# Kernel tuning notes

Measured on AMD Instinct MI355X. Metric: run time of the kernel, lower is better.

The kernel has to match this reference:

```python
import jax, jax.numpy as jnp
import numpy as np

N = 100000        # nodes
E = 3200000       # edges (avg degree 32)
D_IN, D_H, D_OUT = 128, 128, 64
EPS = 1e-5        # BatchNorm eps


def setup_inputs() -> dict:
    key = jax.random.key(0)
    ks = jax.random.split(key, 12)
    s = 0.1
    return {
        "x": jax.random.normal(ks[0], (N, D_IN), jnp.float32),
        "edge_index": jax.random.randint(ks[1], (2, E), 0, N, jnp.int32),
        "W1": jax.random.normal(ks[2], (D_IN, D_H), jnp.float32) * s,
        "b1": jnp.zeros((D_H,), jnp.float32),
        "W2": jax.random.normal(ks[3], (D_H, D_H), jnp.float32) * s,
        "b2": jnp.zeros((D_H,), jnp.float32),
        "W3": jax.random.normal(ks[4], (D_H, D_OUT), jnp.float32) * s,
        "b3": jnp.zeros((D_OUT,), jnp.float32),
        "g1": jnp.ones((D_H,), jnp.float32),
        "be1": jnp.zeros((D_H,), jnp.float32),
        "g2": jnp.ones((D_H,), jnp.float32),
        "be2": jnp.zeros((D_H,), jnp.float32),
    }


def reference(x, edge_index, W1, b1, W2, b2, W3, b3, g1, be1, g2, be2):
    # GCNConv normalization: add self-loops, symmetric deg^-1/2 A deg^-1/2
    loop = jnp.arange(N, dtype=edge_index.dtype)
    src = jnp.concatenate([edge_index[0], loop])   # [E+N]
    dst = jnp.concatenate([edge_index[1], loop])   # [E+N]
    deg = jax.ops.segment_sum(jnp.ones(src.shape, x.dtype), dst, num_segments=N)
    dinv = jnp.where(deg > 0, jax.lax.rsqrt(deg), 0.0)
    norm = (dinv[src] * dinv[dst])[:, None]        # [E+N, 1]

    def conv(h, W, b):
        h = h @ W                                   # dense transform [N, d]
        msg = h[src] * norm                         # gather + scale [E+N, d]
        return jax.ops.segment_sum(msg, dst, num_segments=N) + b

    def bn(h, g, be):  # BatchNorm1d over nodes (batch stats, eval-style dropout)
        m = h.mean(axis=0)
        v = h.var(axis=0)
        return (h - m) * jax.lax.rsqrt(v + EPS) * g + be

    h = jax.nn.relu(bn(conv(x, W1, b1), g1, be1))
    h = jax.nn.relu(bn(conv(h, W2, b2), g2, be2))
    h = conv(h, W3, b3)
    return jax.nn.softmax(h, axis=1)
```

## Files before the change

kernel.cpp:

```cpp
#include <hip/hip_runtime.h>
#include <hip/hip_fp16.h>

constexpr int   NN   = 100000;
constexpr int   NE   = 3200000;
constexpr float BN_EPS = 1e-5f;

constexpr int MG_B  = (NN / 32 + 3) / 4;
constexpr int NB    = (NN + 127) / 128;
constexpr int HB    = 256;
constexpr int CHUNK = NE / HB;
constexpr int BKT_CAP = 5120;
constexpr int IDXW = 512;
constexpr int NPAN = 8;

typedef _Float16 half8 __attribute__((ext_vector_type(8)));
typedef _Float16 h2v   __attribute__((ext_vector_type(2)));
typedef float    floatx16 __attribute__((ext_vector_type(16)));
typedef float    floatx8  __attribute__((ext_vector_type(8)));
typedef int      intx4   __attribute__((ext_vector_type(4)));


__device__ __forceinline__ void acc8_fdot2(floatx8& acc, half8 h) {
  h2v* p = (h2v*)&h;
  const h2v LO = {(_Float16)1.f, (_Float16)0.f};
  const h2v HI = {(_Float16)0.f, (_Float16)1.f};
#pragma unroll
  for (int j = 0; j < 4; ++j) {
    acc[2*j]   = __builtin_amdgcn_fdot2(p[j], LO, acc[2*j],   false);
    acc[2*j+1] = __builtin_amdgcn_fdot2(p[j], HI, acc[2*j+1], false);
  }
}

__global__ __launch_bounds__(256) void k_wprep_all(const float* __restrict__ W1,
                                                   const float* __restrict__ W2,
                                                   const float* __restrict__ W3,
                                                   _Float16* __restrict__ Wt1,
                                                   _Float16* __restrict__ Wt2,
                                                   _Float16* __restrict__ Wt3) {
  int idx = blockIdx.x * 256 + threadIdx.x;
  if (idx < 16384) {
    int k = idx >> 7, n = idx & 127;
    Wt1[n * 128 + k] = (_Float16)W1[idx];
  } else if (idx < 32768) {
    int j = idx - 16384, k = j >> 7, n = j & 127;
    Wt2[n * 128 + k] = (_Float16)W2[j];
  } else if (idx < 40960) {
    int j = idx - 32768, k = j >> 6, n = j & 63;
    Wt3[n * 128 + k] = (_Float16)W3[j];
  }
}

__global__ __launch_bounds__(256) void k_f1(const int* __restrict__ dst,
                                            int* __restrict__ blkhist,
                                            const float* __restrict__ x,
                                            const _Float16* __restrict__ Wt1,
                                            _Float16* __restrict__ C) {
  __shared__ int h[NB];
  if (blockIdx.x < MG_B) {
    int wid  = (blockIdx.x * 256 + threadIdx.x) >> 6;
    int lane = threadIdx.x & 63;
    if (wid >= NN / 32) return;
    const int m = lane & 31;
    const int q = lane >> 5;
    const int row0 = wid * 32;
    const float* Arow = x + (size_t)(row0 + m) * 128 + q * 8;

    floatx16 acc[4] = {};
#pragma unroll
    for (int s = 0; s < 8; ++s) {
      float4 a0 = *(const float4*)(Arow + 16 * s);
      float4 a1 = *(const float4*)(Arow + 16 * s + 4);
      half8 af;
      af[0] = (_Float16)a0.x; af[1] = (_Float16)a0.y;
      af[2] = (_Float16)a0.z; af[3] = (_Float16)a0.w;
      af[4] = (_Float16)a1.x; af[5] = (_Float16)a1.y;
      af[6] = (_Float16)a1.z; af[7] = (_Float16)a1.w;
#pragma unroll
      for (int ct = 0; ct < 4; ++ct) {
        half8 bf = *(const half8*)(Wt1 + (size_t)(ct * 32 + m) * 128 + q * 8 + 16 * s);
        acc[ct] = __builtin_amdgcn_mfma_f32_32x32x16_f16(af, bf, acc[ct], 0, 0, 0);
      }
    }
#pragma unroll
    for (int ct = 0; ct < 4; ++ct) {
      int p = ct * 2 + (m >> 4);
      int off = m & 15;
#pragma unroll
      for (int r = 0; r < 16; ++r) {
        int row = (r & 3) + 8 * (r >> 2) + 4 * q;
        C[((size_t)p * NN + row0 + row) * 16 + off] = (_Float16)acc[ct][r];
      }
    }
  } else {
    int j = blockIdx.x - MG_B;
    int t = threadIdx.x;
    for (int b = t; b < NB; b += 256) h[b] = 0;
    __syncthreads();
    int base = j * CHUNK;
    for (int e = base + t; e < base + CHUNK; e += 256)
      atomicAdd(&h[dst[e] >> 7], 1);
    __syncthreads();
    for (int b = t; b < NB; b += 256) blkhist[j * NB + b] = h[b];
  }
}

__global__ __launch_bounds__(256) void k_scan_bkt_a(const int* __restrict__ blkhist,
                                                    int* __restrict__ blkbase,
                                                    int* __restrict__ total) {
  int wid  = (blockIdx.x * 256 + threadIdx.x) >> 6;
  int lane = threadIdx.x & 63;
  if (wid >= NB) return;
  int i0 = lane * 4;
  int v0 = blkhist[(i0 + 0) * NB + wid];
  int v1 = blkhist[(i0 + 1) * NB + wid];
  int v2 = blkhist[(i0 + 2) * NB + wid];
  int v3 = blkhist[(i0 + 3) * NB + wid];
  int lt = v0 + v1 + v2 + v3;
  int inc = lt;
#pragma unroll
  for (int off = 1; off < 64; off <<= 1) {
    int xx = __shfl_up(inc, off);
    if (lane >= off) inc += xx;
  }
  int exc = inc - lt;
  blkbase[(i0 + 0) * NB + wid] = exc;
  blkbase[(i0 + 1) * NB + wid] = exc + v0;
  blkbase[(i0 + 2) * NB + wid] = exc + v0 + v1;
  blkbase[(i0 + 3) * NB + wid] = exc + v0 + v1 + v2;
  if (lane == 63) total[wid] = inc;
}

__global__ __launch_bounds__(1024) void k_scan_bkt_b(const int* __restrict__ total,
                                                     int* __restrict__ bbase) {
  __shared__ int s[1024];
  int t = threadIdx.x;
  int v = (t < NB) ? total[t] : 0;
  s[t] = v;
  __syncthreads();
  for (int off = 1; off < 1024; off <<= 1) {
    int xx = (t >= off) ? s[t - off] : 0;
    __syncthreads();
    s[t] += xx;
    __syncthreads();
  }
  if (t < NB) bbase[t] = s[t] - v;
  if (t == NB - 1) bbase[NB] = s[t];
}

__global__ __launch_bounds__(256) void k_scatter(const int* __restrict__ ei,
                                                 const int* __restrict__ bbase,
                                                 const int* __restrict__ blkbase,
                                                 int* __restrict__ ebuf) {
  __shared__ int cur[NB];
  int i = blockIdx.x;
  int t = threadIdx.x;
  for (int b = t; b < NB; b += 256) cur[b] = bbase[b] + blkbase[i * NB + b];
  __syncthreads();
  int base = i * CHUNK;
  for (int e = base + t; e < base + CHUNK; e += 256) {
    int s = ei[e];
    int d = ei[NE + e];
    int b = d >> 7;
    int pos = atomicAdd(&cur[b], 1);
    ebuf[pos] = s | ((d & 127) << 17);
  }
}

__global__ __launch_bounds__(256) void k_bucket(const int* __restrict__ bbase,
                                                const int* __restrict__ ebuf,
                                                int* __restrict__ rowptr,
                                                float* __restrict__ dinv,
                                                int* __restrict__ csrc,
                                                _Float16* __restrict__ Hf) {
  __shared__ int degL[128];
  __shared__ int sc[128];
  __shared__ int curL[128];
  __shared__ float dvs[128];
  __shared__ int sorted[BKT_CAP];
  int b = blockIdx.x;
  int t = threadIdx.x;
  int e0 = bbase[b], e1 = bbase[b + 1];
  int cnt = e1 - e0;
  if (t < 128) degL[t] = 0;
  __syncthreads();
  for (int e = e0 + t; e < e1; e += 256)
    atomicAdd(&degL[ebuf[e] >> 17], 1);
  __syncthreads();
  if (t < 128) sc[t] = degL[t];
  __syncthreads();
  for (int off = 1; off < 128; off <<= 1) {
    int xx = 0;
    if (t < 128 && t >= off) xx = sc[t - off];
    __syncthreads();
    if (t < 128) sc[t] += xx;
    __syncthreads();
  }
  if (t < 128) {
    int node = b * 128 + t;
    float dv = 0.f;
    if (node < NN) {
      int d = degL[t];
      int exc = sc[t] - d;
      rowptr[node] = e0 + exc;
      dv = rsqrtf((float)(d + 1));
      dinv[node] = dv;
      curL[t] = exc;
    }
    dvs[t] = dv;
  }
  if (b == NB - 1 && t == 0) rowptr[NN] = NE;
  __syncthreads();
  if (cnt <= BKT_CAP) {
    for (int e = e0 + t; e < e1; e += 256) {
      int p = ebuf[e];
      int pos = atomicAdd(&curL[p >> 17], 1);
      sorted[pos] = p & 0x1FFFF;
    }
    __syncthreads();
    for (int i = t; i < cnt; i += 256) csrc[e0 + i] = sorted[i];
  } else {
    for (int e = e0 + t; e < e1; e += 256) {
      int p = ebuf[e];
      int pos = atomicAdd(&curL[p >> 17], 1);
      csrc[e0 + pos] = p & 0x1FFFF;
    }
  }
  int node = b * 128 + (t >> 1);
  if (node < NN) {
    float dv = dvs[t >> 1];
    size_t base = (size_t)node * 16 + (t & 1) * 8;
#pragma unroll
    for (int k = 0; k < NPAN; ++k) {
      size_t a = (size_t)k * ((size_t)NN * 16) + base;
      half8 h = *(const half8*)(Hf + a);
#pragma unroll
      for (int j = 0; j < 8; ++j) h[j] = (_Float16)((float)h[j] * dv);
      *(half8*)(Hf + a) = h;
    }
  }
}

template <int BN_, bool POUT>
__global__ __launch_bounds__(256) void k_mgemm(const _Float16* __restrict__ A,
                                               const _Float16* __restrict__ Wt,
                                               const float* __restrict__ scale,
                                               const float* __restrict__ shift,
                                               const float* __restrict__ dinv,
                                               _Float16* __restrict__ C) {
  constexpr int NCT = BN_ / 32;
  int wid  = (blockIdx.x * 256 + threadIdx.x) >> 6;
  int lane = threadIdx.x & 63;
  if (wid >= NN / 32) return;
  const int m = lane & 31;
  const int q = lane >> 5;
  const int row0 = wid * 32;

  const _Float16* Abase = A + (size_t)(row0 + m) * 16 + q * 8;

  floatx16 acc[NCT] = {};

#pragma unroll
  for (int s = 0; s < 8; ++s) {
    half8 raw = *(const half8*)(Abase + (size_t)s * ((size_t)NN * 16));
    int k0 = 16 * s + q * 8;
    half8 af;
#pragma unroll
    for (int j = 0; j < 8; ++j) {
      float a = fmaxf(fmaf((float)raw[j], scale[k0 + j], shift[k0 + j]), 0.f);
      af[j] = (_Float16)a;
    }
#pragma unroll
    for (int ct = 0; ct < NCT; ++ct) {
      half8 bf = *(const half8*)(Wt + (size_t)(ct * 32 + m) * 128 + q * 8 + 16 * s);
      acc[ct] = __builtin_amdgcn_mfma_f32_32x32x16_f16(af, bf, acc[ct], 0, 0, 0);
    }
  }

#pragma unroll
  for (int ct = 0; ct < NCT; ++ct) {
    int p = ct * 2 + (m >> 4);
    int off = m & 15;
#pragma unroll
    for (int r = 0; r < 16; ++r) {
      int row = (r & 3) + 8 * (r >> 2) + 4 * q;
      float dv = dinv[row0 + row];
      _Float16 val = (_Float16)(acc[ct][r] * dv);
      if (POUT)
        C[((size_t)p * NN + row0 + row) * 16 + off] = val;
      else
        C[(size_t)(row0 + row) * BN_ + ct * 32 + m] = val;
    }
  }
}

__global__ __launch_bounds__(256) void k_agg128p(const _Float16* __restrict__ Hp,
                                                 const float* __restrict__ dinv,
                                                 const int* __restrict__ rowptr,
                                                 const int* __restrict__ srcs,
                                                 _Float16* __restrict__ outp) {
  __shared__ int sidx[4][IDXW];
  int p  = blockIdx.x & 7;
  int nb = blockIdx.x >> 3;
  int t  = threadIdx.x;
  int w    = t >> 6;
  int lane = t & 63;
  int nid  = lane >> 4;
  int slot = (lane >> 1) & 7;
  int half = lane & 1;
  int node = nb * 16 + w * 4 + nid;

  int beg = rowptr[node];
  int end = rowptr[node + 1];
  int w0   = __shfl(beg, 0);
  int wend = __shfl(end, 63);
  int cnt  = wend - w0;
  int* my = sidx[w];
  bool fits = (cnt <= IDXW);
  if (fits)
    for (int i = lane; i < cnt; i += 64) my[i] = srcs[w0 + i];

  int deg = end - beg;
  int nit = (deg + 7) >> 3;
  int mx = nit;
  mx = max(mx, __shfl_xor(mx, 16));
  mx = max(mx, __shfl_xor(mx, 32));

  const _Float16* base = Hp + (size_t)p * ((size_t)NN * 16) + half * 8;
  int lo = beg - w0;
  floatx8 acc = {};
  if (slot == 0) {
    half8 h = *(const half8*)(base + (size_t)node * 16);
    acc8_fdot2(acc, h);
  }

  int it = 0;
  for (; it + 2 <= mx; it += 2) {
    int j0 = it * 8 + slot;
    int j1 = j0 + 8;
    bool v0 = j0 < deg;
    bool v1 = j1 < deg;
    if (v0) {
      int r0 = fits ? my[lo + j0] : srcs[beg + j0];
      half8 h0 = *(const half8*)(base + (size_t)r0 * 16);
      acc8_fdot2(acc, h0);
    }
    if (v1) {
      int r1 = fits ? my[lo + j1] : srcs[beg + j1];
      half8 h1 = *(const half8*)(base + (size_t)r1 * 16);
      acc8_fdot2(acc, h1);
    }
  }
  for (; it < mx; ++it) {
    int j0 = it * 8 + slot;
    if (j0 < deg) {
      int r0 = fits ? my[lo + j0] : srcs[beg + j0];
      half8 h0 = *(const half8*)(base + (size_t)r0 * 16);
      acc8_fdot2(acc, h0);
    }
  }

#pragma unroll
  for (int k = 0; k < 8; ++k) {
    acc[k] += __shfl_xor(acc[k], 2);
    acc[k] += __shfl_xor(acc[k], 4);
    acc[k] += __shfl_xor(acc[k], 8);
  }
  if (slot == 0) {
    float di = dinv[node];
    __half2 o[4];
#pragma unroll
    for (int j = 0; j < 4; ++j)
      o[j] = __floats2half2_rn(acc[2 * j] * di, acc[2 * j + 1] * di);
    *(intx4*)(outp + ((size_t)p * NN + node) * 16 + half * 8) = *(const intx4*)o;
  }
}

__global__ __launch_bounds__(256) void k_agg64_softmax(const __half* __restrict__ H,
                                                       const float* __restrict__ dinv,
                                                       const int* __restrict__ rowptr,
                                                       const int* __restrict__ srcs,
                                                       const float* __restrict__ b3,
                                                       float* __restrict__ out) {
  int wid  = (blockIdx.x * 256 + threadIdx.x) >> 6;
  int lane = threadIdx.x & 63;
  if (wid >= NN) return;
  const int g  = lane >> 3;
  const int sl = lane & 7;
  const _Float16* Hb = (const _Float16*)H + (size_t)sl * 8;
  floatx8 acc = {};
  if (g == 0) {
    half8 h = *(const half8*)(Hb + (size_t)wid * 64);
    acc8_fdot2(acc, h);
  }
  int beg = rowptr[wid], end = rowptr[wid + 1];
  int n = end - beg;
  int chunk = (n + 7) >> 3;
  int e  = beg + g * chunk; if (e > end) e = end;
  int ce = e + chunk;       if (ce > end) ce = end;
  for (; e + 4 <= ce; e += 4) {
    int s0 = srcs[e + 0], s1 = srcs[e + 1];
    int s2 = srcs[e + 2], s3 = srcs[e + 3];
    half8 h0 = *(const half8*)(Hb + (size_t)s0 * 64);
    half8 h1 = *(const half8*)(Hb + (size_t)s1 * 64);
    half8 h2 = *(const half8*)(Hb + (size_t)s2 * 64);
    half8 h3 = *(const half8*)(Hb + (size_t)s3 * 64);
    acc8_fdot2(acc, h0);
    acc8_fdot2(acc, h1);
    acc8_fdot2(acc, h2);
    acc8_fdot2(acc, h3);
  }
  for (; e < ce; ++e) {
    half8 h0 = *(const half8*)(Hb + (size_t)srcs[e] * 64);
    acc8_fdot2(acc, h0);
  }
#pragma unroll
  for (int j = 0; j < 8; ++j) {
    acc[j] += __shfl_xor(acc[j], 8);
    acc[j] += __shfl_xor(acc[j], 16);
    acc[j] += __shfl_xor(acc[j], 32);
  }
  float di = dinv[wid];
  float4 bA = *(const float4*)(b3 + sl * 8);
  float4 bB = *(const float4*)(b3 + sl * 8 + 4);
  float v[8];
  v[0] = acc[0] * di + bA.x; v[1] = acc[1] * di + bA.y;
  v[2] = acc[2] * di + bA.z; v[3] = acc[3] * di + bA.w;
  v[4] = acc[4] * di + bB.x; v[5] = acc[5] * di + bB.y;
  v[6] = acc[6] * di + bB.z; v[7] = acc[7] * di + bB.w;
  float m = v[0];
#pragma unroll
  for (int j = 1; j < 8; ++j) m = fmaxf(m, v[j]);
  m = fmaxf(m, __shfl_xor(m, 1));
  m = fmaxf(m, __shfl_xor(m, 2));
  m = fmaxf(m, __shfl_xor(m, 4));
  float s = 0.f;
#pragma unroll
  for (int j = 0; j < 8; ++j) { v[j] = __expf(v[j] - m); s += v[j]; }
  s += __shfl_xor(s, 1);
  s += __shfl_xor(s, 2);
  s += __shfl_xor(s, 4);
  float inv = 1.0f / s;
  if (g == 0) {
    float4 oA = {v[0] * inv, v[1] * inv, v[2] * inv, v[3] * inv};
    float4 oB = {v[4] * inv, v[5] * inv, v[6] * inv, v[7] * inv};
    *(float4*)(out + (size_t)wid * 64 + sl * 8)     = oA;
    *(float4*)(out + (size_t)wid * 64 + sl * 8 + 4) = oB;
  }
}

__global__ __launch_bounds__(256) void k_stats(const __half2* __restrict__ H2,
                                               float* __restrict__ S1,
                                               float* __restrict__ S2) {
  int t = threadIdx.x;
  int cp = t & 63;
  int r = t >> 6;
  const __half2* Pb = H2 + (size_t)(cp >> 3) * ((size_t)NN * 8) + (cp & 7);
  float2 s1 = {0.f, 0.f}, s2 = {0.f, 0.f};
  for (int row = blockIdx.x * 4 + r; row < NN; row += gridDim.x * 4) {
    float2 v = __half22float2(Pb[(size_t)row * 8]);
    s1.x += v.x; s1.y += v.y;
    s2.x += v.x * v.x; s2.y += v.y * v.y;
  }
  __shared__ float2 l1[256], l2[256];
  l1[t] = s1; l2[t] = s2;
  __syncthreads();
  if (t < 128) {
    l1[t].x += l1[t+128].x; l1[t].y += l1[t+128].y;
    l2[t].x += l2[t+128].x; l2[t].y += l2[t+128].y;
  }
  __syncthreads();
  if (t < 64) {
    float2 a1 = l1[t], b1 = l1[t+64];
    float2 a2 = l2[t], b2 = l2[t+64];
    atomicAdd(&S1[2*cp+0], a1.x + b1.x);
    atomicAdd(&S1[2*cp+1], a1.y + b1.y);
    atomicAdd(&S2[2*cp+0], a2.x + b2.x);
    atomicAdd(&S2[2*cp+1], a2.y + b2.y);
  }
}

__global__ void k_finalize(const float* __restrict__ S1, const float* __restrict__ S2,
                           const float* __restrict__ g,  const float* __restrict__ be,
                           float* __restrict__ scale,    float* __restrict__ shift) {
  int t = threadIdx.x;
  float mean = S1[t] * (1.0f / NN);
  float var  = S2[t] * (1.0f / NN) - mean * mean;
  float is   = rsqrtf(var + BN_EPS);
  float sc   = g[t] * is;
  scale[t] = sc;
  shift[t] = be[t] - mean * sc;
}

extern "C" void kernel_launch(void* const* d_in, const int* in_sizes, int n_in,
                              void* d_out, int out_size, void* d_ws, size_t ws_size,
                              hipStream_t stream) {
  (void)in_sizes; (void)n_in; (void)out_size; (void)ws_size;
  const float* x   = (const float*)d_in[0];
  const int*   ei  = (const int*)d_in[1];
  const float* W1  = (const float*)d_in[2];
  const float* W2  = (const float*)d_in[4];
  const float* W3  = (const float*)d_in[6];
  const float* b3  = (const float*)d_in[7];
  const float* g1  = (const float*)d_in[8];
  const float* be1 = (const float*)d_in[9];
  const float* g2  = (const float*)d_in[10];
  const float* be2 = (const float*)d_in[11];
  float* out = (float*)d_out;

  char* ws = (char*)d_ws;
  size_t off = 0;
  auto take = [&](size_t bytes) -> char* {
    char* p = ws + off;
    off = (off + bytes + 255) & ~(size_t)255;
    return p;
  };
  float* S1a    = (float*)take(128 * 4);
  float* S2a    = (float*)take(128 * 4);
  float* S1b    = (float*)take(128 * 4);
  float* S2b    = (float*)take(128 * 4);
  size_t zero_bytes = off;
  float* scale1 = (float*)take(128 * 4);
  float* shift1 = (float*)take(128 * 4);
  float* scale2 = (float*)take(128 * 4);
  float* shift2 = (float*)take(128 * 4);
  float* dinv   = (float*)take((size_t)NN * 4);
  int*   rowptr = (int*)  take((size_t)(NN + 1) * 4);
  int*   bbase  = (int*)  take((size_t)(NB + 1) * 4);
  int*   total  = (int*)  take((size_t)NB * 4);
  int*   blkhist= (int*)  take((size_t)HB * NB * 4);
  int*   blkbase= (int*)  take((size_t)HB * NB * 4);
  int*   ebuf   = (int*)  take((size_t)NE * 4);
  int*   csrc   = (int*)  take((size_t)NE * 4);
  _Float16* Wt1 = (_Float16*)take((size_t)128 * 128 * 2);
  _Float16* Wt2 = (_Float16*)take((size_t)128 * 128 * 2);
  _Float16* Wt3 = (_Float16*)take((size_t)64 * 128 * 2);
  _Float16* Hf  = (_Float16*)take((size_t)NN * 128 * 2);
  _Float16* hB  = (_Float16*)take((size_t)NN * 128 * 2);

  (void)hipMemsetAsync(d_ws, 0, zero_bytes, stream);

  const int mgB  = MG_B;
  const int aggB = (NN + 3) / 4;
  const int aggPB = NPAN * (NN / 16);
  const int scanAB = (NB + 3) / 4;

  k_wprep_all<<<160, 256, 0, stream>>>(W1, W2, W3, Wt1, Wt2, Wt3);

  k_f1<<<MG_B + HB, 256, 0, stream>>>(ei + NE, blkhist, x, Wt1, Hf);

  k_scan_bkt_a<<<scanAB, 256, 0, stream>>>(blkhist, blkbase, total);
  k_scan_bkt_b<<<1, 1024, 0, stream>>>(total, bbase);
  k_scatter<<<HB, 256, 0, stream>>>(ei, bbase, blkbase, ebuf);
  k_bucket<<<NB, 256, 0, stream>>>(bbase, ebuf, rowptr, dinv, csrc, Hf);

  k_agg128p<<<aggPB, 256, 0, stream>>>(Hf, dinv, rowptr, csrc, hB);
  k_stats<<<1024, 256, 0, stream>>>((const __half2*)hB, S1a, S2a);
  k_finalize<<<1, 128, 0, stream>>>(S1a, S2a, g1, be1, scale1, shift1);

  k_mgemm<128, true><<<mgB, 256, 0, stream>>>(hB, Wt2, scale1, shift1, dinv, Hf);
  k_agg128p<<<aggPB, 256, 0, stream>>>(Hf, dinv, rowptr, csrc, hB);
  k_stats<<<1024, 256, 0, stream>>>((const __half2*)hB, S1b, S2b);
  k_finalize<<<1, 128, 0, stream>>>(S1b, S2b, g2, be2, scale2, shift2);

  k_mgemm<64, false><<<mgB, 256, 0, stream>>>(hB, Wt3, scale2, shift2, dinv, Hf);
  k_agg64_softmax<<<aggB, 256, 0, stream>>>((const __half*)Hf, dinv, rowptr, csrc, b3, out);
}
```

Before: 741.2 us.

## Assign eight nodes per wave in panel aggregation with contiguous per-slot edge ranges

The 128-wide panel aggregation kernel now maps 8 nodes per wavefront with 4 edge slots each, down from 4 nodes with 8 slots, and halves the grid. Each slot walks a contiguous chunk of the node's edge list with a 4-way unrolled gather, replacing the interleaved strided loop. This removes the wave-wide max-iteration loop and one shuffle reduction stage, and gives more independent loads in flight per lane. In exchange, load balance within a node is coarser and more edge indices share the per-wave shared-memory buffer, so more waves may fall back to global index reads.

```diff
diff --git a/kernel.cpp b/kernel.cpp
--- a/kernel.cpp
+++ b/kernel.cpp
@@ -304,13 +304,14 @@
   int t  = threadIdx.x;
   int w    = t >> 6;
   int lane = t & 63;
-  int nid  = lane >> 4;
-  int slot = (lane >> 1) & 7;
+  int nid  = lane >> 3;
+  int slot = (lane >> 1) & 3;
   int half = lane & 1;
-  int node = nb * 16 + w * 4 + nid;
+  int node = nb * 32 + w * 8 + nid;
 
   int beg = rowptr[node];
   int end = rowptr[node + 1];
+  int deg = end - beg;
   int w0   = __shfl(beg, 0);
   int wend = __shfl(end, 63);
   int cnt  = wend - w0;
@@ -319,42 +320,51 @@
   if (fits)
     for (int i = lane; i < cnt; i += 64) my[i] = srcs[w0 + i];
 
-  int deg = end - beg;
-  int nit = (deg + 7) >> 3;
-  int mx = nit;
-  mx = max(mx, __shfl_xor(mx, 16));
-  mx = max(mx, __shfl_xor(mx, 32));
+  int q  = (deg + 3) >> 2;
+  int e0 = slot * q; if (e0 > deg) e0 = deg;
+  int e1 = e0 + q;   if (e1 > deg) e1 = deg;
 
   const _Float16* base = Hp + (size_t)p * ((size_t)NN * 16) + half * 8;
-  int lo = beg - w0;
   floatx8 acc = {};
   if (slot == 0) {
     half8 h = *(const half8*)(base + (size_t)node * 16);
     acc8_fdot2(acc, h);
   }
 
-  int it = 0;
-  for (; it + 2 <= mx; it += 2) {
-    int j0 = it * 8 + slot;
-    int j1 = j0 + 8;
-    bool v0 = j0 < deg;
-    bool v1 = j1 < deg;
-    if (v0) {
-      int r0 = fits ? my[lo + j0] : srcs[beg + j0];
+  if (fits) {
+    const int* idx = my + (beg - w0);
+    int e = e0;
+    for (; e + 4 <= e1; e += 4) {
+      int r0 = idx[e], r1 = idx[e + 1], r2 = idx[e + 2], r3 = idx[e + 3];
       half8 h0 = *(const half8*)(base + (size_t)r0 * 16);
+      half8 h1 = *(const half8*)(base + (size_t)r1 * 16);
+      half8 h2 = *(const half8*)(base + (size_t)r2 * 16);
+      half8 h3 = *(const half8*)(base + (size_t)r3 * 16);
       acc8_fdot2(acc, h0);
-    }
-    if (v1) {
-      int r1 = fits ? my[lo + j1] : srcs[beg + j1];
+      acc8_fdot2(acc, h1);
+      acc8_fdot2(acc, h2);
+      acc8_fdot2(acc, h3);
+    }
+    for (; e < e1; ++e) {
+      half8 h0 = *(const half8*)(base + (size_t)idx[e] * 16);
+      acc8_fdot2(acc, h0);
+    }
+  } else {
+    const int* idx = srcs + beg;
+    int e = e0;
+    for (; e + 4 <= e1; e += 4) {
+      int r0 = idx[e], r1 = idx[e + 1], r2 = idx[e + 2], r3 = idx[e + 3];
+      half8 h0 = *(const half8*)(base + (size_t)r0 * 16);
       half8 h1 = *(const half8*)(base + (size_t)r1 * 16);
+      half8 h2 = *(const half8*)(base + (size_t)r2 * 16);
+      half8 h3 = *(const half8*)(base + (size_t)r3 * 16);
+      acc8_fdot2(acc, h0);
       acc8_fdot2(acc, h1);
-    }
-  }
-  for (; it < mx; ++it) {
-    int j0 = it * 8 + slot;
-    if (j0 < deg) {
-      int r0 = fits ? my[lo + j0] : srcs[beg + j0];
-      half8 h0 = *(const half8*)(base + (size_t)r0 * 16);
+      acc8_fdot2(acc, h2);
+      acc8_fdot2(acc, h3);
+    }
+    for (; e < e1; ++e) {
+      half8 h0 = *(const half8*)(base + (size_t)idx[e] * 16);
       acc8_fdot2(acc, h0);
     }
   }
@@ -363,7 +373,6 @@
   for (int k = 0; k < 8; ++k) {
     acc[k] += __shfl_xor(acc[k], 2);
     acc[k] += __shfl_xor(acc[k], 4);
-    acc[k] += __shfl_xor(acc[k], 8);
   }
   if (slot == 0) {
     float di = dinv[node];
@@ -541,7 +550,7 @@
 
   const int mgB  = MG_B;
   const int aggB = (NN + 3) / 4;
-  const int aggPB = NPAN * (NN / 16);
+  const int aggPB = NPAN * (NN / 32);
   const int scanAB = (NB + 3) / 4;
 
   k_wprep_all<<<160, 256, 0, stream>>>(W1, W2, W3, Wt1, Wt2, Wt3);
```

Result: faster. 712.1 us (-3.9%).
